# Kernel optimization log

Measured on AMD Instinct MI355X. Metric: run time of the kernel, lower is better.

The kernel has to match this reference:

```python
import jax, jax.numpy as jnp
import numpy as np
import math

HEAD_DIM = 64
N_NEWTON_ITER = 6


def _top_k_sum_selection(T, select_number, mask):
    # T: [B,H,N,D]; mask: [B,N] int (True/1 => masked out for selection, per source)
    B, H, N, D = T.shape
    big = jnp.finfo(T.dtype).max
    # select_type == 'sum' -> non-absolute row sums over feature dim, excluding token 0
    somme = jnp.sum(T[:, :, 1:, :], axis=-1)                      # [B,H,N-1]
    somme = jnp.where(mask[:, None, 1:].astype(bool), -big, somme)
    top = jax.lax.top_k(somme, select_number - 1)[1] + 1          # [B,H,M-1]
    top = jnp.concatenate(
        [top, jnp.zeros((B, H, 1), dtype=top.dtype)], axis=-1)    # always keep token 0
    index = jnp.sort(top, axis=-1)                                 # [B,H,M]
    nt = jnp.take_along_axis(T, index[..., None], axis=2)          # [B,H,M,D]
    return nt, index


def _m_matrix_composition(C, r_index):
    # C: [B,H,N,M]; r_index: [B,H,M] -> gather selected rows -> [B,H,M,M]
    return jnp.take_along_axis(C, r_index[..., None], axis=2)


def _iterative_inv(mat, n_iter=N_NEWTON_ITER):
    M = mat.shape[-1]
    I = jnp.eye(M, dtype=mat.dtype)
    Km = mat
    # init_option == 'original': global max of column sums
    V = (1.0 / jnp.max(jnp.sum(Km, axis=-2))) * jnp.swapaxes(Km, -1, -2)
    for _ in range(n_iter):
        KV = jnp.matmul(Km, V)
        V = jnp.matmul(0.25 * V,
                       13.0 * I - jnp.matmul(KV, 15.0 * I - jnp.matmul(KV, 7.0 * I - KV)))
    return V


def setup_inputs() -> dict:
    key = jax.random.key(0)
    k1, k2, k3, k4 = jax.random.split(key, 4)
    B, H, N, D = 4, 8, 4096, 64
    return {
        "Q": jax.random.normal(k1, (B, H, N, D), dtype=jnp.float32),
        "K": jax.random.normal(k2, (B, H, N, D), dtype=jnp.float32),
        "V": jax.random.normal(k3, (B, H, N, D), dtype=jnp.float32),
        "mask": jax.random.randint(k4, (B, N), 0, 2, dtype=jnp.int32),
        "select_number": 64,
    }


def reference(Q, K, V, mask, select_number):
    big = jnp.finfo(Q.dtype).max
    Qs = Q / math.sqrt(HEAD_DIM)
    nc, _ = _top_k_sum_selection(K, select_number, mask)           # [B,H,M,D]
    nr, r_index = _top_k_sum_selection(Qs, select_number, mask)    # [B,H,M,D]
    c = jnp.einsum('bhnd,bhmd->bhnm', Qs, nc)                      # [B,H,N,M]
    r = jnp.einsum('bhmd,bhnd->bhmn', nr, K)                       # [B,H,M,N]
    # forward path fills where ~mask (mask==0 => masked)
    r = jnp.where(mask[:, None, None, :].astype(bool), r, -big)
    kernel_1 = jax.nn.softmax(c, axis=-1)                          # [B,H,N,M]
    u = _m_matrix_composition(kernel_1, r_index)                   # [B,H,M,M]
    kernel_3 = jax.nn.softmax(r, axis=-1)                          # [B,H,M,N]
    kernel_2_inv = _iterative_inv(u)                               # [B,H,M,M]
    X = jnp.matmul(kernel_1, jnp.matmul(kernel_2_inv, jnp.matmul(kernel_3, V)))
    return X
```

## Files before the change

### kernel.cpp

```cpp
#include <hip/hip_runtime.h>
#include <float.h>

#define BB 4
#define HH 8
#define BHN 32
#define NTOK 4096
#define DD 64
#define MM 64
#define PAD 68
#define GPART 16

typedef _Float16 f16;
typedef __attribute__((ext_vector_type(4))) _Float16 f16x4;
typedef __attribute__((ext_vector_type(8))) _Float16 f16x8;
typedef __attribute__((ext_vector_type(4))) float f32x4;

union V8U { f16x8 v; f16x4 q[2]; };

__device__ __forceinline__ void fsplit(float v, f16* h, f16* l) {
  f16 hh = (f16)v;
  *h = hh;
  *l = (f16)(v - (float)hh);
}

__device__ __forceinline__ f32x4 mm2(f16x8 a0, f16x8 a1, f16x8 b0, f16x8 b1) {
  f32x4 c = {0.f, 0.f, 0.f, 0.f};
  c = __builtin_amdgcn_mfma_f32_16x16x32_f16(a0, b0, c, 0, 0, 0);
  c = __builtin_amdgcn_mfma_f32_16x16x32_f16(a1, b1, c, 0, 0, 0);
  return c;
}

template<int LDA, int LDB>
__device__ __forceinline__ void mm_acc(float acc[4][4],
    const float (*A)[LDA], const float (*B)[LDB], int ti, int tj) {
  #pragma unroll
  for (int k4 = 0; k4 < 16; ++k4) {
    float a[4][4], b[4][4];
    #pragma unroll
    for (int x = 0; x < 4; ++x) {
      float4 t = *(const float4*)&A[ti*4+x][k4*4];
      a[x][0]=t.x; a[x][1]=t.y; a[x][2]=t.z; a[x][3]=t.w;
    }
    #pragma unroll
    for (int kk = 0; kk < 4; ++kk) {
      float4 t = *(const float4*)&B[k4*4+kk][tj*4];
      b[kk][0]=t.x; b[kk][1]=t.y; b[kk][2]=t.z; b[kk][3]=t.w;
    }
    #pragma unroll
    for (int kk = 0; kk < 4; ++kk)
      #pragma unroll
      for (int x = 0; x < 4; ++x)
        #pragma unroll
        for (int y = 0; y < 4; ++y)
          acc[x][y] = fmaf(a[x][kk], b[kk][y], acc[x][y]);
  }
}

__global__ __launch_bounds__(256) void k_somme(const float* __restrict__ Kg,
    const float* __restrict__ Qg, const int* __restrict__ mask,
    float* __restrict__ somK, float* __restrict__ somQ) {
  int tid = threadIdx.x;
  int lane = tid & 63;
  long grow = (long)blockIdx.x * 16 + (tid >> 6) * 4 + (lane >> 4);
  int which = grow >= (long)(BHN * NTOK);
  long row = which ? grow - (long)BHN * NTOK : grow;
  int n = (int)(row & (NTOK - 1));
  int bh = (int)(row >> 12);
  int b = bh >> 3;
  const float* src = which ? Qg : Kg;
  float4 v = *((const float4*)(src + row * DD) + (lane & 15));
  float s = v.x + v.y + v.z + v.w;
  s += __shfl_xor(s, 1); s += __shfl_xor(s, 2);
  s += __shfl_xor(s, 4); s += __shfl_xor(s, 8);
  if ((lane & 15) == 0) {
    float out = (n == 0 || mask[b * NTOK + n] != 0) ? -FLT_MAX : s;
    (which ? somQ : somK)[row] = out;
  }
}

__global__ __launch_bounds__(256) void k_select(const float* __restrict__ Kg,
    const float* __restrict__ Qg, const float* __restrict__ somK,
    const float* __restrict__ somQ, float* __restrict__ nc, float* __restrict__ nr) {
  int bh = blockIdx.x;
  int which = blockIdx.y;
  __shared__ unsigned int keys[NTOK];
  __shared__ unsigned int wb[4][256];
  __shared__ int wsum[4];
  __shared__ int wsumB[4];
  __shared__ int sh_bin, sh_need;
  __shared__ int sel[MM];
  int tid = threadIdx.x, wave = tid >> 6, lane = tid & 63;
  const float* som = (which ? somQ : somK) + (long)bh * NTOK;
  for (int i = tid; i < NTOK; i += 256) {
    float f = som[i];
    unsigned int u = __float_as_uint(f);
    u = (u & 0x80000000u) ? ~u : (u | 0x80000000u);
    keys[i] = (i == 0) ? 0u : u;
  }
  unsigned int pref = 0; int need = MM - 1;
  for (int pass = 0; pass < 4; ++pass) {
    int shift = 24 - pass * 8;
    unsigned int pm = (pass == 0) ? 0u : (0xFFFFFFFFu << (32 - 8 * pass));
    unsigned int* wbf = (unsigned int*)wb;
    wbf[tid] = 0; wbf[tid + 256] = 0; wbf[tid + 512] = 0; wbf[tid + 768] = 0;
    __syncthreads();
    for (int i = tid; i < NTOK; i += 256) {
      unsigned int k = keys[i];
      if ((k & pm) == pref) atomicAdd(&wb[wave][(k >> shift) & 255], 1u);
    }
    __syncthreads();
    int binr = 255 - tid;
    int cnt = (int)(wb[0][binr] + wb[1][binr] + wb[2][binr] + wb[3][binr]);
    int v = cnt;
    #pragma unroll
    for (int d = 1; d < 64; d <<= 1) {
      int t = __shfl_up(v, d);
      if (lane >= d) v += t;
    }
    if (lane == 63) wsum[wave] = v;
    __syncthreads();
    int off = 0;
    #pragma unroll
    for (int w = 0; w < 4; ++w) off += (w < wave) ? wsum[w] : 0;
    v += off;
    int above = v - cnt;
    if (v >= need && above < need) { sh_bin = binr; sh_need = need - above; }
    __syncthreads();
    pref |= ((unsigned int)sh_bin) << shift;
    need = sh_need;
  }
  unsigned int thr = pref;

  int base = tid * 16;
  int ctie = 0;
  #pragma unroll
  for (int j = 0; j < 16; ++j) ctie += (keys[base + j] == thr);
  int v2 = ctie;
  #pragma unroll
  for (int d = 1; d < 64; d <<= 1) {
    int t = __shfl_up(v2, d);
    if (lane >= d) v2 += t;
  }
  if (lane == 63) wsum[wave] = v2;
  __syncthreads();
  int offt = 0;
  #pragma unroll
  for (int w = 0; w < 4; ++w) offt += (w < wave) ? wsum[w] : 0;
  int tie_excl = v2 + offt - ctie;

  int tieoff = tie_excl, cnt2 = 0;
  #pragma unroll
  for (int j = 0; j < 16; ++j) {
    unsigned int k = keys[base + j];
    int f = (k > thr) ? 1 : 0;
    if (k == thr) { f = (tieoff < need) ? 1 : 0; ++tieoff; }
    if (base + j == 0) f = 1;
    cnt2 += f;
  }
  int v3 = cnt2;
  #pragma unroll
  for (int d = 1; d < 64; d <<= 1) {
    int t = __shfl_up(v3, d);
    if (lane >= d) v3 += t;
  }
  if (lane == 63) wsumB[wave] = v3;
  __syncthreads();
  int offc = 0;
  #pragma unroll
  for (int w = 0; w < 4; ++w) offc += (w < wave) ? wsumB[w] : 0;
  int o = v3 + offc - cnt2;
  tieoff = tie_excl;
  #pragma unroll
  for (int j = 0; j < 16; ++j) {
    unsigned int k = keys[base + j];
    int f = (k > thr) ? 1 : 0;
    if (k == thr) { f = (tieoff < need) ? 1 : 0; ++tieoff; }
    if (base + j == 0) f = 1;
    if (f) sel[o++] = base + j;
  }
  __syncthreads();

  const float* src = which ? Qg : Kg;
  float* dst = (which ? nr : nc) + (long)bh * MM * DD;
  float scale = which ? 0.125f : 1.0f;
  for (int e = tid; e < MM * 16; e += 256) {
    int i = e >> 4, d4 = e & 15;
    float4 v = *(const float4*)&src[((long)bh * NTOK + sel[i]) * DD + d4 * 4];
    v.x *= scale; v.y *= scale; v.z *= scale; v.w *= scale;
    *(float4*)&dst[i * DD + d4 * 4] = v;
  }
}

__global__ __launch_bounds__(256) void k_u(const float* __restrict__ nc,
    const float* __restrict__ nr, float* __restrict__ u, float* __restrict__ smax) {
  int bh = blockIdx.x, tid = threadIdx.x, ti = tid >> 4, tj = tid & 15;
  __shared__ float A[MM][PAD];
  __shared__ float BT[DD][MM];
  __shared__ float cs[4][MM];
  for (int e = tid; e < 1024; e += 256) {
    int m = e >> 4, d4 = e & 15;
    *(float4*)&A[m][d4*4] = *(const float4*)&nr[(long)bh*MM*DD + m*DD + d4*4];
    float4 c = *(const float4*)&nc[(long)bh*MM*DD + m*DD + d4*4];
    BT[d4*4+0][m] = c.x; BT[d4*4+1][m] = c.y; BT[d4*4+2][m] = c.z; BT[d4*4+3][m] = c.w;
  }
  __syncthreads();
  float acc[4][4] = {};
  mm_acc<PAD, MM>(acc, A, BT, ti, tj);
  float e_[4][4];
  #pragma unroll
  for (int x = 0; x < 4; ++x)
    #pragma unroll
    for (int y = 0; y < 4; ++y) e_[x][y] = expf(acc[x][y]);
  float rsx[4];
  #pragma unroll
  for (int x = 0; x < 4; ++x) {
    rsx[x] = e_[x][0] + e_[x][1] + e_[x][2] + e_[x][3];
    rsx[x] += __shfl_xor(rsx[x], 1); rsx[x] += __shfl_xor(rsx[x], 2);
    rsx[x] += __shfl_xor(rsx[x], 4); rsx[x] += __shfl_xor(rsx[x], 8);
  }
  float cp[4] = {0.f, 0.f, 0.f, 0.f};
  #pragma unroll
  for (int x = 0; x < 4; ++x) {
    float inv = 1.f / rsx[x];
    float v0 = e_[x][0]*inv, v1 = e_[x][1]*inv, v2 = e_[x][2]*inv, v3 = e_[x][3]*inv;
    cp[0] += v0; cp[1] += v1; cp[2] += v2; cp[3] += v3;
    float4 o; o.x = v0; o.y = v1; o.z = v2; o.w = v3;
    *(float4*)&u[(long)bh*MM*MM + (ti*4+x)*MM + tj*4] = o;
  }
  #pragma unroll
  for (int y = 0; y < 4; ++y) {
    cp[y] += __shfl_xor(cp[y], 16);
    cp[y] += __shfl_xor(cp[y], 32);
  }
  if (((tid >> 4) & 3) == 0) {
    #pragma unroll
    for (int y = 0; y < 4; ++y) cs[tid >> 6][tj*4 + y] = cp[y];
  }
  __syncthreads();
  if (tid < 64) {
    float tot = cs[0][tid] + cs[1][tid] + cs[2][tid] + cs[3][tid];
    for (int off = 32; off; off >>= 1) tot = fmaxf(tot, __shfl_xor(tot, off));
    if (tid == 0) smax[bh] = tot;
  }
}

__device__ void newton_dev(char* smem, const float* __restrict__ u,
    const float* __restrict__ smax, float* __restrict__ vinv, int bh) {
  f16 (*VT_h)[72] = (f16(*)[72])(smem);
  f16 (*Vr_h)[72] = (f16(*)[72])(smem + 9216);
  f16 (*PT_h)[72] = (f16(*)[72])(smem + 18432);
  f16 (*PT_l)[72] = (f16(*)[72])(smem + 27648);
  f16 (*RT_h)[72] = (f16(*)[72])(smem + 36864);
  f16 (*RT_l)[72] = (f16(*)[72])(smem + 46080);
  int tid = threadIdx.x;
  int wave = tid >> 6, lane = tid & 63;
  int wr = wave >> 1, wc = wave & 1;
  int lm = lane & 15, hi = lane >> 4;

  float gmx = smax[0];
  #pragma unroll
  for (int i = 1; i < 32; ++i) gmx = fmaxf(gmx, smax[i]);
  float c0 = 1.0f / gmx;

  const float* pu = u + (long)bh * MM * MM;
  for (int e = tid; e < 4096; e += 512) {
    int i = e >> 6, j = e & 63;
    f16 h = (f16)(pu[e] * c0);
    VT_h[i][j] = h;
    Vr_h[j][i] = h;
  }
  f16x8 kb_h[2], kb_l[2];
  {
    const float* p = pu + (wr*16 + lm) * 64;
    float kv[16];
    *(float4*)&kv[0]  = *(const float4*)(p + hi*8);
    *(float4*)&kv[4]  = *(const float4*)(p + hi*8 + 4);
    *(float4*)&kv[8]  = *(const float4*)(p + 32 + hi*8);
    *(float4*)&kv[12] = *(const float4*)(p + 36 + hi*8);
    #pragma unroll
    for (int j = 0; j < 8; ++j) {
      f16 h, l;
      fsplit(kv[j], &h, &l);     kb_h[0][j] = h; kb_l[0][j] = l;
      fsplit(kv[8+j], &h, &l);   kb_h[1][j] = h; kb_l[1][j] = l;
    }
  }
  __syncthreads();

  for (int it = 0; it < 6; ++it) {
    const bool last = (it == 5);

    f32x4 st[4];
    #pragma unroll
    for (int g = 0; g < 4; ++g) {
      f16x8 a0 = *(const f16x8*)&VT_h[g*16 + lm][hi*8];
      f16x8 a1 = *(const f16x8*)&VT_h[g*16 + lm][32 + hi*8];
      f32x4 c = mm2(a0, a1, kb_h[0], kb_h[1]);
      if (last) {
        c = __builtin_amdgcn_mfma_f32_16x16x32_f16(a0, kb_l[0], c, 0, 0, 0);
        c = __builtin_amdgcn_mfma_f32_16x16x32_f16(a1, kb_l[1], c, 0, 0, 0);
      }
      st[g] = c;
    }
    f16x8 sa[2];
    #pragma unroll
    for (int g = 0; g < 4; ++g)
      #pragma unroll
      for (int r = 0; r < 4; ++r)
        sa[g >> 1][(g & 1)*4 + r] = (f16)st[g][r];
    #pragma unroll
    for (int g = 0; g < 4; ++g) {
      if ((g >> 1) == wc) {
        #pragma unroll
        for (int r = 0; r < 4; ++r) {
          int i = g*16 + hi*4 + r, j = wr*16 + lm;
          float pv = (i == j ? 7.f : 0.f) - st[g][r];
          if (last) {
            f16 h, l; fsplit(pv, &h, &l);
            PT_h[i][j] = h; PT_l[i][j] = l;
          } else {
            PT_h[i][j] = (f16)pv;
          }
        }
      }
    }
    __syncthreads();

    #pragma unroll
    for (int cc2 = 0; cc2 < 2; ++cc2) {
      int cc = wc*2 + cc2;
      V8U bh0, bh1;
      bh0.q[0] = *(const f16x4*)&PT_h[cc*16 + lm][hi*4];
      bh0.q[1] = *(const f16x4*)&PT_h[cc*16 + lm][16 + hi*4];
      bh1.q[0] = *(const f16x4*)&PT_h[cc*16 + lm][32 + hi*4];
      bh1.q[1] = *(const f16x4*)&PT_h[cc*16 + lm][48 + hi*4];
      f32x4 a = mm2(sa[0], sa[1], bh0.v, bh1.v);
      if (last) {
        V8U bl0, bl1;
        bl0.q[0] = *(const f16x4*)&PT_l[cc*16 + lm][hi*4];
        bl0.q[1] = *(const f16x4*)&PT_l[cc*16 + lm][16 + hi*4];
        bl1.q[0] = *(const f16x4*)&PT_l[cc*16 + lm][32 + hi*4];
        bl1.q[1] = *(const f16x4*)&PT_l[cc*16 + lm][48 + hi*4];
        a = __builtin_amdgcn_mfma_f32_16x16x32_f16(sa[0], bl0.v, a, 0, 0, 0);
        a = __builtin_amdgcn_mfma_f32_16x16x32_f16(sa[1], bl1.v, a, 0, 0, 0);
      }
      f16x4 wh, wl;
      #pragma unroll
      for (int r = 0; r < 4; ++r) {
        int row = wr*16 + hi*4 + r, col = cc*16 + lm;
        float rv = (row == col ? 15.f : 0.f) - a[r];
        if (last) { f16 h, l; fsplit(rv, &h, &l); wh[r] = h; wl[r] = l; }
        else wh[r] = (f16)rv;
      }
      *(f16x4*)&RT_h[cc*16 + lm][wr*16 + hi*4] = wh;
      if (last) *(f16x4*)&RT_l[cc*16 + lm][wr*16 + hi*4] = wl;
    }
    __syncthreads();

    #pragma unroll
    for (int cc2 = 0; cc2 < 2; ++cc2) {
      int cc = wc*2 + cc2;
      V8U bh0, bh1;
      bh0.q[0] = *(const f16x4*)&RT_h[cc*16 + lm][hi*4];
      bh0.q[1] = *(const f16x4*)&RT_h[cc*16 + lm][16 + hi*4];
      bh1.q[0] = *(const f16x4*)&RT_h[cc*16 + lm][32 + hi*4];
      bh1.q[1] = *(const f16x4*)&RT_h[cc*16 + lm][48 + hi*4];
      f32x4 a = mm2(sa[0], sa[1], bh0.v, bh1.v);
      if (last) {
        V8U bl0, bl1;
        bl0.q[0] = *(const f16x4*)&RT_l[cc*16 + lm][hi*4];
        bl0.q[1] = *(const f16x4*)&RT_l[cc*16 + lm][16 + hi*4];
        bl1.q[0] = *(const f16x4*)&RT_l[cc*16 + lm][32 + hi*4];
        bl1.q[1] = *(const f16x4*)&RT_l[cc*16 + lm][48 + hi*4];
        a = __builtin_amdgcn_mfma_f32_16x16x32_f16(sa[0], bl0.v, a, 0, 0, 0);
        a = __builtin_amdgcn_mfma_f32_16x16x32_f16(sa[1], bl1.v, a, 0, 0, 0);
      }
      f16x4 wh, wl;
      #pragma unroll
      for (int r = 0; r < 4; ++r) {
        int row = wr*16 + hi*4 + r, col = cc*16 + lm;
        float wv = (row == col ? 13.f : 0.f) - a[r];
        if (last) { f16 h, l; fsplit(wv, &h, &l); wh[r] = h; wl[r] = l; }
        else wh[r] = (f16)wv;
      }
      *(f16x4*)&PT_h[cc*16 + lm][wr*16 + hi*4] = wh;
      if (last) *(f16x4*)&PT_l[cc*16 + lm][wr*16 + hi*4] = wl;
    }
    __syncthreads();

    f16x8 vh0 = *(const f16x8*)&Vr_h[wr*16 + lm][hi*8];
    f16x8 vh1 = *(const f16x8*)&Vr_h[wr*16 + lm][32 + hi*8];
    #pragma unroll
    for (int cc2 = 0; cc2 < 2; ++cc2) {
      int cc = wc*2 + cc2;
      f16x8 wh0 = *(const f16x8*)&PT_h[cc*16 + lm][hi*8];
      f16x8 wh1 = *(const f16x8*)&PT_h[cc*16 + lm][32 + hi*8];
      f32x4 a = mm2(vh0, vh1, wh0, wh1);
      if (last) {
        f16x8 wl0 = *(const f16x8*)&PT_l[cc*16 + lm][hi*8];
        f16x8 wl1 = *(const f16x8*)&PT_l[cc*16 + lm][32 + hi*8];
        a = __builtin_amdgcn_mfma_f32_16x16x32_f16(vh0, wl0, a, 0, 0, 0);
        a = __builtin_amdgcn_mfma_f32_16x16x32_f16(vh1, wl1, a, 0, 0, 0);
        #pragma unroll
        for (int r = 0; r < 4; ++r)
          vinv[(long)bh*MM*MM + (wr*16 + hi*4 + r)*MM + cc*16 + lm] = 0.25f * a[r];
      } else {
        f16x4 th;
        #pragma unroll
        for (int r = 0; r < 4; ++r) {
          f16 h = (f16)(0.25f * a[r]);
          Vr_h[wr*16 + hi*4 + r][cc*16 + lm] = h;
          th[r] = h;
        }
        *(f16x4*)&VT_h[cc*16 + lm][wr*16 + hi*4] = th;
      }
    }
    __syncthreads();
  }
}

__device__ void w3_dev(char* smem, const float* __restrict__ Kg,
    const float* __restrict__ Vg, const int* __restrict__ maskg,
    const float* __restrict__ nr, float* __restrict__ nump,
    float* __restrict__ denp, int idx) {
  int bh = idx >> 3, grp = idx & 7, b = bh >> 3;
  int tid = threadIdx.x;
  int half = tid >> 8, t = tid & 255;
  f16 (*Ks)[72] = (f16(*)[72])(smem + half * 18432);
  f16 (*Vs)[72] = (f16(*)[72])(smem + half * 18432 + 9216);
  float* kmul = (float*)(smem + 36864) + half * 64;
  int lane = tid & 63;
  int lm = lane & 15, hi = lane >> 4;
  int wv = t >> 6;
  int m0 = wv * 16;
  int gslot = grp * 2 + half;

  f16x8 nrf[2];
  {
    const float* p = nr + (long)bh*MM*DD + (long)(m0 + lm)*DD + hi*8;
    float4 q0 = *(const float4*)p;
    float4 q1 = *(const float4*)(p + 4);
    float4 q2 = *(const float4*)(p + 32);
    float4 q3 = *(const float4*)(p + 36);
    nrf[0][0]=(f16)q0.x; nrf[0][1]=(f16)q0.y; nrf[0][2]=(f16)q0.z; nrf[0][3]=(f16)q0.w;
    nrf[0][4]=(f16)q1.x; nrf[0][5]=(f16)q1.y; nrf[0][6]=(f16)q1.z; nrf[0][7]=(f16)q1.w;
    nrf[1][0]=(f16)q2.x; nrf[1][1]=(f16)q2.y; nrf[1][2]=(f16)q2.z; nrf[1][3]=(f16)q2.w;
    nrf[1][4]=(f16)q3.x; nrf[1][5]=(f16)q3.y; nrf[1][6]=(f16)q3.z; nrf[1][7]=(f16)q3.w;
  }

  f32x4 nacc[4];
  #pragma unroll
  for (int dt = 0; dt < 4; ++dt) nacc[dt] = (f32x4){0.f, 0.f, 0.f, 0.f};
  float dsum = 0.f;

  for (int sc = 0; sc < 4; ++sc) {
    int n0c = (gslot * 4 + sc) * 64;
    if (sc) __syncthreads();
    for (int s = t; s < 1024; s += 256) {
      int row = s >> 4, c4 = s & 15;
      float4 kv = *(const float4*)&Kg[((long)bh*NTOK + n0c + row)*DD + c4*4];
      float4 vv = *(const float4*)&Vg[((long)bh*NTOK + n0c + row)*DD + c4*4];
      f16x4 kk = {(f16)kv.x, (f16)kv.y, (f16)kv.z, (f16)kv.w};
      f16x4 vv4 = {(f16)vv.x, (f16)vv.y, (f16)vv.z, (f16)vv.w};
      *(f16x4*)&Ks[row][c4*4] = kk;
      *(f16x4*)&Vs[row][c4*4] = vv4;
    }
    if (t < 64) kmul[t] = maskg[b * NTOK + n0c + t] ? 1.f : 0.f;
    __syncthreads();

    f32x4 stv[4];
    #pragma unroll
    for (int g = 0; g < 4; ++g) {
      f16x8 a0 = *(const f16x8*)&Ks[g*16 + lm][hi*8];
      f16x8 a1 = *(const f16x8*)&Ks[g*16 + lm][32 + hi*8];
      stv[g] = mm2(a0, a1, nrf[0], nrf[1]);
    }
    f16x8 pa[2];
    #pragma unroll
    for (int g = 0; g < 4; ++g) {
      #pragma unroll
      for (int r = 0; r < 4; ++r) {
        float p = __expf(stv[g][r]) * kmul[g*16 + hi*4 + r];
        dsum += p;
        pa[g >> 1][(g & 1)*4 + r] = (f16)p;
      }
    }
    #pragma unroll
    for (int dt = 0; dt < 4; ++dt) {
      f16x8 vb0, vb1;
      #pragma unroll
      for (int j = 0; j < 8; ++j) {
        int nrow = hi*4 + (j & 3) + 16*(j >> 2);
        vb0[j] = Vs[nrow][dt*16 + lm];
        vb1[j] = Vs[32 + nrow][dt*16 + lm];
      }
      nacc[dt] = __builtin_amdgcn_mfma_f32_16x16x32_f16(pa[0], vb0, nacc[dt], 0, 0, 0);
      nacc[dt] = __builtin_amdgcn_mfma_f32_16x16x32_f16(pa[1], vb1, nacc[dt], 0, 0, 0);
    }
  }
  float* pnum = nump + ((long)bh * GPART + gslot) * (MM * DD);
  #pragma unroll
  for (int dt = 0; dt < 4; ++dt)
    #pragma unroll
    for (int r = 0; r < 4; ++r)
      pnum[(m0 + hi*4 + r)*DD + dt*16 + lm] = nacc[dt][r];
  float d2 = dsum + __shfl_xor(dsum, 16);
  d2 += __shfl_xor(d2, 32);
  if (lane < 16)
    denp[((long)bh * GPART + gslot) * MM + m0 + lane] = d2;
}

__global__ __launch_bounds__(512) void k_mix(const float* __restrict__ u,
    const float* __restrict__ smax, float* __restrict__ vinv,
    const float* __restrict__ Kg, const float* __restrict__ Vg,
    const int* __restrict__ maskg, const float* __restrict__ nr,
    float* __restrict__ nump, float* __restrict__ denp) {
  __shared__ __align__(16) char smem[55296];
  if (blockIdx.x < 32)
    newton_dev(smem, u, smax, vinv, blockIdx.x);
  else
    w3_dev(smem, Kg, Vg, maskg, nr, nump, denp, blockIdx.x - 32);
}

__global__ __launch_bounds__(256) void k_z(const float* __restrict__ vinv,
    const float* __restrict__ nump, const float* __restrict__ denp, float* __restrict__ Zg) {
  int bh = blockIdx.x, tid = threadIdx.x, ti = tid >> 4, tj = tid & 15;
  __shared__ float A[MM][PAD];
  __shared__ float W[MM][MM];
  __shared__ float dn[MM];
  if (tid < 64) {
    float s = 0.f;
    #pragma unroll
    for (int g = 0; g < GPART; ++g) s += denp[((long)bh * GPART + g) * MM + tid];
    dn[tid] = s;
  }
  for (int e = tid; e < 1024; e += 256) {
    int m = e >> 4, d4 = e & 15;
    *(float4*)&A[m][d4*4] = *(const float4*)&vinv[(long)bh*MM*MM + m*MM + d4*4];
  }
  __syncthreads();
  for (int e = tid; e < 1024; e += 256) {
    int m = e >> 4, d4 = e & 15;
    float4 s = {0.f, 0.f, 0.f, 0.f};
    #pragma unroll
    for (int g = 0; g < GPART; ++g) {
      float4 t = *(const float4*)&nump[((long)bh * GPART + g) * (MM*DD) + m*DD + d4*4];
      s.x += t.x; s.y += t.y; s.z += t.z; s.w += t.w;
    }
    float inv = 1.f / dn[m];
    s.x *= inv; s.y *= inv; s.z *= inv; s.w *= inv;
    *(float4*)&W[m][d4*4] = s;
  }
  __syncthreads();
  float acc[4][4] = {};
  mm_acc<PAD, MM>(acc, A, W, ti, tj);
  #pragma unroll
  for (int x = 0; x < 4; ++x) {
    float4 o; o.x = acc[x][0]; o.y = acc[x][1]; o.z = acc[x][2]; o.w = acc[x][3];
    *(float4*)&Zg[(long)bh*MM*DD + (ti*4+x)*DD + tj*4] = o;
  }
}

__global__ __launch_bounds__(256) void k_final(const float* __restrict__ Qg,
    const float* __restrict__ nc, const float* __restrict__ Zg, float* __restrict__ Xg) {
  int bh = blockIdx.x, chunk = blockIdx.y;
  int tid = threadIdx.x;
  int wave = tid >> 6, lane = tid & 63;
  int lm = lane & 15, hi = lane >> 4;
  int n0 = chunk * 64;
  __shared__ f16 Qs[64][72];
  __shared__ f16 Ncs[64][72];
  __shared__ f16 Zs[64][72];
  for (int s = tid; s < 1024; s += 256) {
    int row = s >> 4, c4 = s & 15;
    float4 q = *(const float4*)&Qg[((long)bh*NTOK + n0 + row)*DD + c4*4];
    f16x4 qq = {(f16)(q.x*0.125f), (f16)(q.y*0.125f), (f16)(q.z*0.125f), (f16)(q.w*0.125f)};
    *(f16x4*)&Qs[row][c4*4] = qq;
    float4 cv = *(const float4*)&nc[(long)bh*MM*DD + row*DD + c4*4];
    f16x4 cc = {(f16)cv.x, (f16)cv.y, (f16)cv.z, (f16)cv.w};
    *(f16x4*)&Ncs[row][c4*4] = cc;
    float4 zv = *(const float4*)&Zg[(long)bh*MM*DD + row*DD + c4*4];
    f16x4 zz = {(f16)zv.x, (f16)zv.y, (f16)zv.z, (f16)zv.w};
    *(f16x4*)&Zs[row][c4*4] = zz;
  }
  __syncthreads();

  f16x8 qb0 = *(const f16x8*)&Qs[wave*16 + lm][hi*8];
  f16x8 qb1 = *(const f16x8*)&Qs[wave*16 + lm][32 + hi*8];
  f32x4 stv[4];
  #pragma unroll
  for (int mt = 0; mt < 4; ++mt) {
    f16x8 a0 = *(const f16x8*)&Ncs[mt*16 + lm][hi*8];
    f16x8 a1 = *(const f16x8*)&Ncs[mt*16 + lm][32 + hi*8];
    stv[mt] = mm2(a0, a1, qb0, qb1);
  }
  f16x8 pa[2];
  float dsum = 0.f;
  #pragma unroll
  for (int mt = 0; mt < 4; ++mt) {
    #pragma unroll
    for (int r = 0; r < 4; ++r) {
      float p = __expf(stv[mt][r]);
      dsum += p;
      pa[mt >> 1][(mt & 1)*4 + r] = (f16)p;
    }
  }
  float dtot = dsum + __shfl_xor(dsum, 16);
  dtot += __shfl_xor(dtot, 32);
  f32x4 xacc[4];
  #pragma unroll
  for (int dt = 0; dt < 4; ++dt) {
    f16x8 zb0, zb1;
    #pragma unroll
    for (int j = 0; j < 8; ++j) {
      int mrow = hi*4 + (j & 3) + 16*(j >> 2);
      zb0[j] = Zs[mrow][dt*16 + lm];
      zb1[j] = Zs[32 + mrow][dt*16 + lm];
    }
    f32x4 c = {0.f, 0.f, 0.f, 0.f};
    c = __builtin_amdgcn_mfma_f32_16x16x32_f16(pa[0], zb0, c, 0, 0, 0);
    c = __builtin_amdgcn_mfma_f32_16x16x32_f16(pa[1], zb1, c, 0, 0, 0);
    xacc[dt] = c;
  }
  float rn[4];
  #pragma unroll
  for (int r = 0; r < 4; ++r) rn[r] = 1.f / __shfl(dtot, hi*4 + r);
  #pragma unroll
  for (int dt = 0; dt < 4; ++dt)
    #pragma unroll
    for (int r = 0; r < 4; ++r)
      Xg[((long)bh*NTOK + n0 + wave*16 + hi*4 + r)*DD + dt*16 + lm] = xacc[dt][r] * rn[r];
}

extern "C" void kernel_launch(void* const* d_in, const int* in_sizes, int n_in,
                              void* d_out, int out_size, void* d_ws, size_t ws_size,
                              hipStream_t stream) {
  (void)in_sizes; (void)n_in; (void)out_size; (void)ws_size;
  const float* Qp = (const float*)d_in[0];
  const float* Kp = (const float*)d_in[1];
  const float* Vp = (const float*)d_in[2];
  const int* maskp = (const int*)d_in[3];
  float* out = (float*)d_out;

  float* wsf = (float*)d_ws;
  float* NUMP = wsf;
  float* DENP = NUMP + (long)BHN * GPART * MM * DD;
  float* SMAX = DENP + BHN * GPART * MM;
  float* NC = SMAX + 32;
  float* NR = NC + BHN * MM * DD;
  float* U  = NR + BHN * MM * DD;
  float* VI = U  + BHN * MM * MM;
  float* Zb = VI + BHN * MM * MM;
  float* SK = Zb + BHN * MM * DD;
  float* SQ = SK + BHN * NTOK;

  k_somme<<<16384, 256, 0, stream>>>(Kp, Qp, maskp, SK, SQ);
  k_select<<<dim3(32, 2), 256, 0, stream>>>(Kp, Qp, SK, SQ, NC, NR);
  k_u<<<32, 256, 0, stream>>>(NC, NR, U, SMAX);
  k_mix<<<32 + 256, 512, 0, stream>>>(U, SMAX, VI, Kp, Vp, maskp, NR, NUMP, DENP);
  k_z<<<32, 256, 0, stream>>>(VI, NUMP, DENP, Zb);
  k_final<<<dim3(32, 64), 256, 0, stream>>>(Qp, NC, Zb, out);
}
```

Before: 80.53 us.

## Fuse u-matrix, Newton inverse and Z computation into one kernel with spin flags

Merges the separate k_u and k_z kernels into the mixed Newton/w3 kernel. The 32 Newton blocks now compute their softmax u-matrix in shared memory, share the global column-sum max through an atomicMax plus a grid-level flag spin, and later wait on per-bh counters set by the w3 blocks before computing Z locally. This removes two kernel launches and the global round trips for U, SMAX and VINV. In exchange it relies on all participating blocks being co-resident so the spin waits cannot deadlock, and it grows shared memory per block, which may lower occupancy.

After: 80.14 us (median of 3 runs). Within noise of the previous version (-0.5%).

```diff
diff --git a/kernel.cpp b/kernel.cpp
--- a/kernel.cpp
+++ b/kernel.cpp
@@ -80,9 +80,14 @@
 
 __global__ __launch_bounds__(256) void k_select(const float* __restrict__ Kg,
     const float* __restrict__ Qg, const float* __restrict__ somK,
-    const float* __restrict__ somQ, float* __restrict__ nc, float* __restrict__ nr) {
+    const float* __restrict__ somQ, float* __restrict__ nc, float* __restrict__ nr,
+    unsigned int* __restrict__ sync0) {
   int bh = blockIdx.x;
   int which = blockIdx.y;
+  if (which == 0 && bh == 0 && threadIdx.x == 0) {
+    #pragma unroll
+    for (int i = 0; i < 34; ++i) sync0[i] = 0u;
+  }
   __shared__ unsigned int keys[NTOK];
   __shared__ unsigned int wb[4][256];
   __shared__ int wsum[4];
@@ -191,87 +196,102 @@
   }
 }
 
-__global__ __launch_bounds__(256) void k_u(const float* __restrict__ nc,
-    const float* __restrict__ nr, float* __restrict__ u, float* __restrict__ smax) {
-  int bh = blockIdx.x, tid = threadIdx.x, ti = tid >> 4, tj = tid & 15;
-  __shared__ float A[MM][PAD];
-  __shared__ float BT[DD][MM];
-  __shared__ float cs[4][MM];
-  for (int e = tid; e < 1024; e += 256) {
-    int m = e >> 4, d4 = e & 15;
-    *(float4*)&A[m][d4*4] = *(const float4*)&nr[(long)bh*MM*DD + m*DD + d4*4];
-    float4 c = *(const float4*)&nc[(long)bh*MM*DD + m*DD + d4*4];
-    BT[d4*4+0][m] = c.x; BT[d4*4+1][m] = c.y; BT[d4*4+2][m] = c.z; BT[d4*4+3][m] = c.w;
-  }
-  __syncthreads();
-  float acc[4][4] = {};
-  mm_acc<PAD, MM>(acc, A, BT, ti, tj);
-  float e_[4][4];
-  #pragma unroll
-  for (int x = 0; x < 4; ++x)
-    #pragma unroll
-    for (int y = 0; y < 4; ++y) e_[x][y] = expf(acc[x][y]);
-  float rsx[4];
-  #pragma unroll
-  for (int x = 0; x < 4; ++x) {
-    rsx[x] = e_[x][0] + e_[x][1] + e_[x][2] + e_[x][3];
-    rsx[x] += __shfl_xor(rsx[x], 1); rsx[x] += __shfl_xor(rsx[x], 2);
-    rsx[x] += __shfl_xor(rsx[x], 4); rsx[x] += __shfl_xor(rsx[x], 8);
-  }
-  float cp[4] = {0.f, 0.f, 0.f, 0.f};
-  #pragma unroll
-  for (int x = 0; x < 4; ++x) {
-    float inv = 1.f / rsx[x];
-    float v0 = e_[x][0]*inv, v1 = e_[x][1]*inv, v2 = e_[x][2]*inv, v3 = e_[x][3]*inv;
-    cp[0] += v0; cp[1] += v1; cp[2] += v2; cp[3] += v3;
-    float4 o; o.x = v0; o.y = v1; o.z = v2; o.w = v3;
-    *(float4*)&u[(long)bh*MM*MM + (ti*4+x)*MM + tj*4] = o;
-  }
-  #pragma unroll
-  for (int y = 0; y < 4; ++y) {
-    cp[y] += __shfl_xor(cp[y], 16);
-    cp[y] += __shfl_xor(cp[y], 32);
-  }
-  if (((tid >> 4) & 3) == 0) {
-    #pragma unroll
-    for (int y = 0; y < 4; ++y) cs[tid >> 6][tj*4 + y] = cp[y];
-  }
-  __syncthreads();
-  if (tid < 64) {
-    float tot = cs[0][tid] + cs[1][tid] + cs[2][tid] + cs[3][tid];
-    for (int off = 32; off; off >>= 1) tot = fmaxf(tot, __shfl_xor(tot, off));
-    if (tid == 0) smax[bh] = tot;
-  }
-}
-
-__device__ void newton_dev(char* smem, const float* __restrict__ u,
-    const float* __restrict__ smax, float* __restrict__ vinv, int bh) {
+__device__ void newton_fused(char* smem, const float* __restrict__ nc,
+    const float* __restrict__ nr, unsigned int* __restrict__ scal,
+    unsigned int* __restrict__ uflag, const float* __restrict__ nump,
+    const float* __restrict__ denp, unsigned int* __restrict__ w3cnt,
+    float* __restrict__ Zg, int bh) {
+  int tid = threadIdx.x;
+  float* uL = (float*)(smem + 55296);
+
+  {
+    float (*A)[PAD] = (float(*)[PAD])smem;
+    float (*BT)[MM] = (float(*)[MM])(smem + 17408);
+    float (*cs)[MM] = (float(*)[MM])(smem + 33792);
+    if (tid < 256) {
+      for (int e = tid; e < 1024; e += 256) {
+        int m = e >> 4, d4 = e & 15;
+        *(float4*)&A[m][d4*4] = *(const float4*)&nr[(long)bh*MM*DD + m*DD + d4*4];
+        float4 c = *(const float4*)&nc[(long)bh*MM*DD + m*DD + d4*4];
+        BT[d4*4+0][m] = c.x; BT[d4*4+1][m] = c.y; BT[d4*4+2][m] = c.z; BT[d4*4+3][m] = c.w;
+      }
+    }
+    __syncthreads();
+    if (tid < 256) {
+      int ti = tid >> 4, tj = tid & 15;
+      float acc[4][4] = {};
+      mm_acc<PAD, MM>(acc, A, BT, ti, tj);
+      float e_[4][4];
+      #pragma unroll
+      for (int x = 0; x < 4; ++x)
+        #pragma unroll
+        for (int y = 0; y < 4; ++y) e_[x][y] = expf(acc[x][y]);
+      float rsx[4];
+      #pragma unroll
+      for (int x = 0; x < 4; ++x) {
+        rsx[x] = e_[x][0] + e_[x][1] + e_[x][2] + e_[x][3];
+        rsx[x] += __shfl_xor(rsx[x], 1); rsx[x] += __shfl_xor(rsx[x], 2);
+        rsx[x] += __shfl_xor(rsx[x], 4); rsx[x] += __shfl_xor(rsx[x], 8);
+      }
+      float cp[4] = {0.f, 0.f, 0.f, 0.f};
+      #pragma unroll
+      for (int x = 0; x < 4; ++x) {
+        float inv = 1.f / rsx[x];
+        float v0 = e_[x][0]*inv, v1 = e_[x][1]*inv, v2 = e_[x][2]*inv, v3 = e_[x][3]*inv;
+        cp[0] += v0; cp[1] += v1; cp[2] += v2; cp[3] += v3;
+        float4 o; o.x = v0; o.y = v1; o.z = v2; o.w = v3;
+        *(float4*)&uL[(ti*4+x)*MM + tj*4] = o;
+      }
+      #pragma unroll
+      for (int y = 0; y < 4; ++y) {
+        cp[y] += __shfl_xor(cp[y], 16);
+        cp[y] += __shfl_xor(cp[y], 32);
+      }
+      if (((tid >> 4) & 3) == 0) {
+        #pragma unroll
+        for (int y = 0; y < 4; ++y) cs[tid >> 6][tj*4 + y] = cp[y];
+      }
+    }
+    __syncthreads();
+    if (tid < 64) {
+      float tot = cs[0][tid] + cs[1][tid] + cs[2][tid] + cs[3][tid];
+      for (int off = 32; off; off >>= 1) tot = fmaxf(tot, __shfl_xor(tot, off));
+      if (tid == 0) atomicMax(scal, __float_as_uint(tot));
+    }
+    __syncthreads();
+    if (tid == 0)
+      __hip_atomic_fetch_add(uflag, 1u, __ATOMIC_RELEASE, __HIP_MEMORY_SCOPE_AGENT);
+    if (tid == 0) {
+      while (__hip_atomic_load(uflag, __ATOMIC_ACQUIRE, __HIP_MEMORY_SCOPE_AGENT) < 32u)
+        __builtin_amdgcn_s_sleep(1);
+      unsigned int sv = __hip_atomic_load(scal, __ATOMIC_RELAXED, __HIP_MEMORY_SCOPE_AGENT);
+      cs[0][0] = 1.0f / __uint_as_float(sv);
+    }
+    __syncthreads();
+  }
+  float c0 = ((float(*)[MM])(smem + 33792))[0][0];
+  __syncthreads();
+
   f16 (*VT_h)[72] = (f16(*)[72])(smem);
   f16 (*Vr_h)[72] = (f16(*)[72])(smem + 9216);
   f16 (*PT_h)[72] = (f16(*)[72])(smem + 18432);
   f16 (*PT_l)[72] = (f16(*)[72])(smem + 27648);
   f16 (*RT_h)[72] = (f16(*)[72])(smem + 36864);
   f16 (*RT_l)[72] = (f16(*)[72])(smem + 46080);
-  int tid = threadIdx.x;
+  float (*Vi)[PAD] = (float(*)[PAD])(smem + 36864);
   int wave = tid >> 6, lane = tid & 63;
   int wr = wave >> 1, wc = wave & 1;
   int lm = lane & 15, hi = lane >> 4;
 
-  float gmx = smax[0];
-  #pragma unroll
-  for (int i = 1; i < 32; ++i) gmx = fmaxf(gmx, smax[i]);
-  float c0 = 1.0f / gmx;
-
-  const float* pu = u + (long)bh * MM * MM;
   for (int e = tid; e < 4096; e += 512) {
     int i = e >> 6, j = e & 63;
-    f16 h = (f16)(pu[e] * c0);
+    f16 h = (f16)(uL[e] * c0);
     VT_h[i][j] = h;
     Vr_h[j][i] = h;
   }
   f16x8 kb_h[2], kb_l[2];
   {
-    const float* p = pu + (wr*16 + lm) * 64;
+    const float* p = uL + (wr*16 + lm) * 64;
     float kv[16];
     *(float4*)&kv[0]  = *(const float4*)(p + hi*8);
     *(float4*)&kv[4]  = *(const float4*)(p + hi*8 + 4);
@@ -402,7 +422,7 @@
         a = __builtin_amdgcn_mfma_f32_16x16x32_f16(vh1, wl1, a, 0, 0, 0);
         #pragma unroll
         for (int r = 0; r < 4; ++r)
-          vinv[(long)bh*MM*MM + (wr*16 + hi*4 + r)*MM + cc*16 + lm] = 0.25f * a[r];
+          Vi[wr*16 + hi*4 + r][cc*16 + lm] = 0.25f * a[r];
       } else {
         f16x4 th;
         #pragma unroll
@@ -416,12 +436,50 @@
     }
     __syncthreads();
   }
+
+  if (tid == 0) {
+    while (__hip_atomic_load(&w3cnt[bh], __ATOMIC_ACQUIRE, __HIP_MEMORY_SCOPE_AGENT) < 8u)
+      __builtin_amdgcn_s_sleep(1);
+  }
+  __syncthreads();
+  float (*W)[PAD] = (float(*)[PAD])smem;
+  float* dn = (float*)(smem + 54272);
+  if (tid < 64) {
+    float s = 0.f;
+    #pragma unroll
+    for (int g = 0; g < GPART; ++g) s += denp[((long)bh * GPART + g) * MM + tid];
+    dn[tid] = s;
+  }
+  __syncthreads();
+  for (int e = tid; e < 1024; e += 512) {
+    int m = e >> 4, d4 = e & 15;
+    float4 s = {0.f, 0.f, 0.f, 0.f};
+    #pragma unroll
+    for (int g = 0; g < GPART; ++g) {
+      float4 t = *(const float4*)&nump[((long)bh * GPART + g) * (MM*DD) + m*DD + d4*4];
+      s.x += t.x; s.y += t.y; s.z += t.z; s.w += t.w;
+    }
+    float inv = 1.f / dn[m];
+    s.x *= inv; s.y *= inv; s.z *= inv; s.w *= inv;
+    *(float4*)&W[m][d4*4] = s;
+  }
+  __syncthreads();
+  if (tid < 256) {
+    int ti = tid >> 4, tj = tid & 15;
+    float acc[4][4] = {};
+    mm_acc<PAD, PAD>(acc, Vi, W, ti, tj);
+    #pragma unroll
+    for (int x = 0; x < 4; ++x) {
+      float4 o; o.x = acc[x][0]; o.y = acc[x][1]; o.z = acc[x][2]; o.w = acc[x][3];
+      *(float4*)&Zg[(long)bh*MM*DD + (ti*4+x)*DD + tj*4] = o;
+    }
+  }
 }
 
 __device__ void w3_dev(char* smem, const float* __restrict__ Kg,
     const float* __restrict__ Vg, const int* __restrict__ maskg,
     const float* __restrict__ nr, float* __restrict__ nump,
-    float* __restrict__ denp, int idx) {
+    float* __restrict__ denp, unsigned int* __restrict__ w3cnt, int idx) {
   int bh = idx >> 3, grp = idx & 7, b = bh >> 3;
   int tid = threadIdx.x;
   int half = tid >> 8, t = tid & 255;
@@ -507,57 +565,23 @@
   d2 += __shfl_xor(d2, 32);
   if (lane < 16)
     denp[((long)bh * GPART + gslot) * MM + m0 + lane] = d2;
-}
-
-__global__ __launch_bounds__(512) void k_mix(const float* __restrict__ u,
-    const float* __restrict__ smax, float* __restrict__ vinv,
+  __syncthreads();
+  if (tid == 0)
+    __hip_atomic_fetch_add(&w3cnt[bh], 1u, __ATOMIC_RELEASE, __HIP_MEMORY_SCOPE_AGENT);
+}
+
+__global__ __launch_bounds__(512, 4) void k_fuse(
+    const float* __restrict__ nc, const float* __restrict__ nr,
+    unsigned int* __restrict__ scal, unsigned int* __restrict__ uflag,
     const float* __restrict__ Kg, const float* __restrict__ Vg,
-    const int* __restrict__ maskg, const float* __restrict__ nr,
-    float* __restrict__ nump, float* __restrict__ denp) {
-  __shared__ __align__(16) char smem[55296];
+    const int* __restrict__ maskg,
+    float* __restrict__ nump, float* __restrict__ denp,
+    unsigned int* __restrict__ w3cnt, float* __restrict__ Zg) {
+  __shared__ __align__(16) char smem[71680];
   if (blockIdx.x < 32)
-    newton_dev(smem, u, smax, vinv, blockIdx.x);
+    newton_fused(smem, nc, nr, scal, uflag, nump, denp, w3cnt, Zg, blockIdx.x);
   else
-    w3_dev(smem, Kg, Vg, maskg, nr, nump, denp, blockIdx.x - 32);
-}
-
-__global__ __launch_bounds__(256) void k_z(const float* __restrict__ vinv,
-    const float* __restrict__ nump, const float* __restrict__ denp, float* __restrict__ Zg) {
-  int bh = blockIdx.x, tid = threadIdx.x, ti = tid >> 4, tj = tid & 15;
-  __shared__ float A[MM][PAD];
-  __shared__ float W[MM][MM];
-  __shared__ float dn[MM];
-  if (tid < 64) {
-    float s = 0.f;
-    #pragma unroll
-    for (int g = 0; g < GPART; ++g) s += denp[((long)bh * GPART + g) * MM + tid];
-    dn[tid] = s;
-  }
-  for (int e = tid; e < 1024; e += 256) {
-    int m = e >> 4, d4 = e & 15;
-    *(float4*)&A[m][d4*4] = *(const float4*)&vinv[(long)bh*MM*MM + m*MM + d4*4];
-  }
-  __syncthreads();
-  for (int e = tid; e < 1024; e += 256) {
-    int m = e >> 4, d4 = e & 15;
-    float4 s = {0.f, 0.f, 0.f, 0.f};
-    #pragma unroll
-    for (int g = 0; g < GPART; ++g) {
-      float4 t = *(const float4*)&nump[((long)bh * GPART + g) * (MM*DD) + m*DD + d4*4];
-      s.x += t.x; s.y += t.y; s.z += t.z; s.w += t.w;
-    }
-    float inv = 1.f / dn[m];
-    s.x *= inv; s.y *= inv; s.z *= inv; s.w *= inv;
-    *(float4*)&W[m][d4*4] = s;
-  }
-  __syncthreads();
-  float acc[4][4] = {};
-  mm_acc<PAD, MM>(acc, A, W, ti, tj);
-  #pragma unroll
-  for (int x = 0; x < 4; ++x) {
-    float4 o; o.x = acc[x][0]; o.y = acc[x][1]; o.z = acc[x][2]; o.w = acc[x][3];
-    *(float4*)&Zg[(long)bh*MM*DD + (ti*4+x)*DD + tj*4] = o;
-  }
+    w3_dev(smem, Kg, Vg, maskg, nr, nump, denp, w3cnt, blockIdx.x - 32);
 }
 
 __global__ __launch_bounds__(256) void k_final(const float* __restrict__ Qg,
@@ -644,19 +668,20 @@
   float* wsf = (float*)d_ws;
   float* NUMP = wsf;
   float* DENP = NUMP + (long)BHN * GPART * MM * DD;
-  float* SMAX = DENP + BHN * GPART * MM;
-  float* NC = SMAX + 32;
+  unsigned int* SYNC = (unsigned int*)(DENP + BHN * GPART * MM);
+  float* NC = (float*)(SYNC + 64);
   float* NR = NC + BHN * MM * DD;
-  float* U  = NR + BHN * MM * DD;
-  float* VI = U  + BHN * MM * MM;
-  float* Zb = VI + BHN * MM * MM;
+  float* Zb = NR + BHN * MM * DD;
   float* SK = Zb + BHN * MM * DD;
   float* SQ = SK + BHN * NTOK;
 
+  unsigned int* SCAL = SYNC;
+  unsigned int* UFLAG = SYNC + 1;
+  unsigned int* W3CNT = SYNC + 2;
+
   k_somme<<<16384, 256, 0, stream>>>(Kp, Qp, maskp, SK, SQ);
-  k_select<<<dim3(32, 2), 256, 0, stream>>>(Kp, Qp, SK, SQ, NC, NR);
-  k_u<<<32, 256, 0, stream>>>(NC, NR, U, SMAX);
-  k_mix<<<32 + 256, 512, 0, stream>>>(U, SMAX, VI, Kp, Vp, maskp, NR, NUMP, DENP);
-  k_z<<<32, 256, 0, stream>>>(VI, NUMP, DENP, Zb);
+  k_select<<<dim3(32, 2), 256, 0, stream>>>(Kp, Qp, SK, SQ, NC, NR, SYNC);
+  k_fuse<<<32 + 256, 512, 0, stream>>>(NC, NR, SCAL, UFLAG, Kp, Vp, maskp,
+                                       NUMP, DENP, W3CNT, Zb);
   k_final<<<dim3(32, 64), 256, 0, stream>>>(Qp, NC, Zb, out);
 }
```
